# Performance work log

Hardware: AMD Instinct MI355X
Metric: run time of the kernel (lower is better)

The kernel has to match this reference:

```python
import jax, jax.numpy as jnp
import numpy as np

N = 32768      # total nodes
B = 64         # graphs
NPG = 512      # nodes per graph
E = 524288     # edges (avg degree 16)
H = 4          # heads
Fh = 64        # per-head dim
C = H * Fh     # 256
FIN = 128
RATIO = 0.5


def gat(x, src, dst, W, a_src, a_dst, bias, n_nodes):
    # PyG GATConv: linear -> add self-loops -> edge softmax over dst -> scatter-add
    h = (x @ W).reshape(n_nodes, H, Fh)
    loop = jnp.arange(n_nodes)
    s = jnp.concatenate([src, loop])
    d = jnp.concatenate([dst, loop])
    es = jnp.sum(h * a_src, axis=-1)  # [N,H]
    ed = jnp.sum(h * a_dst, axis=-1)  # [N,H]
    e = jax.nn.leaky_relu(es[s] + ed[d], 0.2)  # [E+N,H]
    m = jax.ops.segment_max(e, d, num_segments=n_nodes)
    ex = jnp.exp(e - m[d])
    den = jax.ops.segment_sum(ex, d, num_segments=n_nodes)
    alpha = ex / (den[d] + 1e-16)  # [E+N,H]
    out = jax.ops.segment_sum(alpha[:, :, None] * h[s], d, num_segments=n_nodes)
    return out.reshape(n_nodes, C) + bias


def pool(x, sw, sb, tw, tb, n_graphs, n_per):
    # equal-size graphs -> per-graph top-k as a batched top_k
    k = max(1, int(n_per * RATIO))
    scores = jax.nn.sigmoid(x @ sw + sb)[:, 0].reshape(n_graphs, n_per)
    _, idx = jax.lax.top_k(scores, k)  # [B,k]
    xb = x.reshape(n_graphs, n_per, x.shape[-1])
    sel = jnp.take_along_axis(xb, idx[:, :, None], axis=1)
    sel = sel.reshape(n_graphs * k, x.shape[-1])
    return sel @ tw + tb, k


def setup_inputs() -> dict:
    key = jax.random.key(0)
    ks = jax.random.split(key, 24)
    x = jax.random.normal(ks[0], (N, FIN), dtype=jnp.float32)
    # within-graph random edges
    gbase = jnp.repeat(jnp.arange(B, dtype=jnp.int32) * NPG, E // B)
    src = gbase + jax.random.randint(ks[1], (E,), 0, NPG)
    dst = gbase + jax.random.randint(ks[2], (E,), 0, NPG)
    edge_index = jnp.stack([src, dst]).astype(jnp.int32)
    batch = jnp.repeat(jnp.arange(B, dtype=jnp.int32), NPG)
    def lin(k, fi, fo):
        return jax.random.normal(k, (fi, fo), dtype=jnp.float32) / np.sqrt(fi)
    inp = dict(x=x, edge_index=edge_index, batch=batch)
    inp["W1"] = lin(ks[3], FIN, C)
    inp["a_src1"] = jax.random.normal(ks[4], (H, Fh), jnp.float32) / np.sqrt(Fh)
    inp["a_dst1"] = jax.random.normal(ks[5], (H, Fh), jnp.float32) / np.sqrt(Fh)
    inp["b1"] = jnp.zeros((C,), jnp.float32)
    inp["W2"] = lin(ks[6], C, C)
    inp["a_src2"] = jax.random.normal(ks[7], (H, Fh), jnp.float32) / np.sqrt(Fh)
    inp["a_dst2"] = jax.random.normal(ks[8], (H, Fh), jnp.float32) / np.sqrt(Fh)
    inp["b2"] = jnp.zeros((C,), jnp.float32)
    inp["p1_sw"] = lin(ks[9], C, 1)
    inp["p1_sb"] = jnp.zeros((1,), jnp.float32)
    inp["p1_tw"] = lin(ks[10], C, C)
    inp["p1_tb"] = jnp.zeros((C,), jnp.float32)
    inp["p2_sw"] = lin(ks[11], C, 1)
    inp["p2_sb"] = jnp.zeros((1,), jnp.float32)
    inp["p2_tw"] = lin(ks[12], C, C)
    inp["p2_tb"] = jnp.zeros((C,), jnp.float32)
    inp["c1w"] = lin(ks[13], C, 64)
    inp["c1b"] = jnp.zeros((64,), jnp.float32)
    inp["c2w"] = lin(ks[14], 64, 2)
    inp["c2b"] = jnp.zeros((2,), jnp.float32)
    return inp


def reference(x, edge_index, batch, W1, a_src1, a_dst1, b1, W2, a_src2, a_dst2, b2,
              p1_sw, p1_sb, p1_tw, p1_tb, p2_sw, p2_sb, p2_tw, p2_tb,
              c1w, c1b, c2w, c2b):
    src, dst = edge_index[0], edge_index[1]
    h = jax.nn.elu(gat(x, src, dst, W1, a_src1, a_dst1, b1, N))
    h = jax.nn.elu(gat(h, src, dst, W2, a_src2, a_dst2, b2, N))
    # pool1 then pool2 (edge_index after pooling is never consumed by the output path)
    h, k1 = pool(h, p1_sw, p1_sb, p1_tw, p1_tb, B, NPG)
    h, k2 = pool(h, p2_sw, p2_sb, p2_tw, p2_tb, B, k1)
    g = h.reshape(B, k2, C).mean(axis=1)  # global mean pool per graph
    g = jax.nn.relu(g @ c1w + c1b)
    g = g @ c2w + c2b
    return jax.nn.log_softmax(g, axis=1)
```

## Files before the change

### kernel.cpp

```cpp
#include <hip/hip_runtime.h>
#include <hip/hip_bf16.h>
#include <hip/hip_fp16.h>
#include <math.h>

constexpr int NN  = 32768;
constexpr int BG  = 64;
constexpr int NPG = 512;
constexpr int EG  = 524288;
constexpr int EPG = EG / BG;
constexpr int HH  = 4;
constexpr int FH  = 64;
constexpr int CC  = 256;
constexpr int FIN = 128;
constexpr int KP1 = 256;
constexpr int KP2 = 128;
constexpr int NS  = 4;

typedef __attribute__((ext_vector_type(8))) short short8;
typedef __attribute__((ext_vector_type(4))) float f32x4;
typedef __attribute__((ext_vector_type(2))) float f32x2v;

__device__ inline float leaky02(float v) { return v > 0.0f ? v : 0.2f * v; }

__device__ inline unsigned short f2bf(float v) {
    __hip_bfloat16 h = __float2bfloat16(v);
    return *(unsigned short*)&h;
}
__device__ inline float bf2f(unsigned short u) {
    __hip_bfloat16 h;
    *(unsigned short*)&h = u;
    return __bfloat162float(h);
}
__device__ inline void split2(float v, unsigned short& hi, unsigned short& lo) {
    hi = f2bf(v);
    lo = f2bf(v - bf2f(hi));
}
__device__ inline void split8(const float* p, short8& hi, short8& lo) {
    const float4 f0 = *(const float4*)p;
    const float4 f1 = *(const float4*)(p + 4);
    unsigned short h, l;
    split2(f0.x, h, l); hi[0] = (short)h; lo[0] = (short)l;
    split2(f0.y, h, l); hi[1] = (short)h; lo[1] = (short)l;
    split2(f0.z, h, l); hi[2] = (short)h; lo[2] = (short)l;
    split2(f0.w, h, l); hi[3] = (short)h; lo[3] = (short)l;
    split2(f1.x, h, l); hi[4] = (short)h; lo[4] = (short)l;
    split2(f1.y, h, l); hi[5] = (short)h; lo[5] = (short)l;
    split2(f1.z, h, l); hi[6] = (short)h; lo[6] = (short)l;
    split2(f1.w, h, l); hi[7] = (short)h; lo[7] = (short)l;
}

__device__ inline unsigned short f2h(float v) {
    __half h = __float2half(v);
    return *(unsigned short*)&h;
}
__device__ inline float h2f(unsigned short u) {
    __half h;
    *(unsigned short*)&h = u;
    return __half2float(h);
}

__device__ inline unsigned int fmap(float v) {
    unsigned int b = __float_as_uint(v);
    return (b & 0x80000000u) ? ~b : (b | 0x80000000u);
}

__device__ inline void acc8h(const unsigned short* p, float a, f32x2v* acc) {
    const uint4 u = *(const uint4*)p;
    const __half2* hp = (const __half2*)&u;
    f32x2v av; av[0] = a; av[1] = a;
#pragma unroll
    for (int i = 0; i < 4; ++i) {
        const float2 f = __half22float2(hp[i]);
        f32x2v fv; fv[0] = f.x; fv[1] = f.y;
        acc[i] = __builtin_elementwise_fma(fv, av, acc[i]);
    }
}

__global__ __launch_bounds__(1024) void setup_k(
        const int* __restrict__ src, const int* __restrict__ dst,
        int* __restrict__ rowp, int* __restrict__ esrc,
        const float* __restrict__ tw1, const float* __restrict__ sw2,
        const float* __restrict__ tb1, const float* __restrict__ sb2,
        float* __restrict__ w12, float* __restrict__ b12,
        const float* __restrict__ tw2, const float* __restrict__ c1w,
        const float* __restrict__ tb2, float* __restrict__ T,
        float* __restrict__ bc2,
        const float* __restrict__ W1, const float* __restrict__ W2,
        unsigned short* __restrict__ w1ph, unsigned short* __restrict__ w1pl,
        unsigned short* __restrict__ w2ph, unsigned short* __restrict__ w2pl,
        const float* __restrict__ x,
        unsigned short* __restrict__ xph, unsigned short* __restrict__ xpl) {
    __shared__ int lcnt[NPG];
    __shared__ int wsum[8];
    const int b = blockIdx.x;
    const int t = threadIdx.x;
    if (b < BG) {
        const int g = b;
        const int ebase = g * EPG;
        const int nbase = g * NPG;
        if (t < NPG) lcnt[t] = 0;
        __syncthreads();
        int ds[EPG / 1024];
#pragma unroll
        for (int j = 0; j < EPG / 1024; ++j) {
            ds[j] = dst[ebase + t + 1024 * j] - nbase;
            atomicAdd(&lcnt[ds[j]], 1);
        }
        __syncthreads();
        int c = 0, sInc = 0;
        if (t < NPG) {
            c = lcnt[t];
            sInc = c;
#pragma unroll
            for (int o = 1; o < 64; o <<= 1) {
                int v = __shfl_up(sInc, o);
                if ((t & 63) >= o) sInc += v;
            }
            if ((t & 63) == 63) wsum[t >> 6] = sInc;
        }
        __syncthreads();
        if (t < 8) {
            int v = wsum[t];
            int s = v;
#pragma unroll
            for (int o = 1; o < 8; o <<= 1) {
                int u2 = __shfl_up(s, o, 8);
                if (t >= o) s += u2;
            }
            wsum[t] = s - v;
        }
        __syncthreads();
        if (t < NPG) {
            const int ex = sInc - c + wsum[t >> 6];
            rowp[nbase + t] = ebase + ex;
            lcnt[t] = ex;
        }
        if (g == BG - 1 && t == 0) rowp[NN] = EG;
        __syncthreads();
#pragma unroll
        for (int j = 0; j < EPG / 1024; ++j) {
            int p = atomicAdd(&lcnt[ds[j]], 1);
            esrc[ebase + p] = src[ebase + t + 1024 * j];
        }
        return;
    }
    const int pb = b - BG;
    if (pb >= 114) {
        const size_t idx = ((size_t)(pb - 114) * 1024 + t) * 8;
        short8 hi, lo;
        split8(x + idx, hi, lo);
        *(short8*)(xph + idx) = hi;
        *(short8*)(xpl + idx) = lo;
        return;
    }
    if (t >= 256) return;
    if (pb < 66) {
        if (pb == 0) {
            float s = 0.0f;
            for (int o = 0; o < CC; ++o) s += tw1[t * CC + o] * sw2[o];
            w12[t] = s;
            if (t == 0) {
                float bb = 0.0f;
                for (int o = 0; o < CC; ++o) bb += tb1[o] * sw2[o];
                *b12 = bb + sb2[0];
            }
        } else if (pb < 65) {
            const int r = (pb - 1) * 4 + (t >> 6);
            const int cth = t & 63;
            float s = 0.0f;
            for (int j = 0; j < CC; ++j) s = fmaf(tw2[r * CC + j], c1w[j * 64 + cth], s);
            T[r * 64 + cth] = s;
        } else if (t < 64) {
            float s = 0.0f;
            for (int j = 0; j < CC; ++j) s = fmaf(tb2[j], c1w[j * 64 + t], s);
            bc2[t] = s;
        }
    } else {
        const int idx = (pb - 66) * 256 + t;
        if (idx < 4096) {
            const int nt = idx >> 8, rem = idx & 255;
            const int kg = rem >> 6, l = rem & 63;
            const int n = nt * 16 + (l & 15);
            const int kb = kg * 32 + (l >> 4) * 8;
            unsigned short h[8], lo[8];
#pragma unroll
            for (int j = 0; j < 8; ++j) split2(W1[(kb + j) * CC + n], h[j], lo[j]);
#pragma unroll
            for (int j = 0; j < 8; ++j) {
                w1ph[(size_t)idx * 8 + j] = h[j];
                w1pl[(size_t)idx * 8 + j] = lo[j];
            }
        } else {
            const int i2 = idx - 4096;
            const int nt = i2 >> 9, rem = i2 & 511;
            const int kg = rem >> 6, l = rem & 63;
            const int n = nt * 16 + (l & 15);
            const int kb = kg * 32 + (l >> 4) * 8;
            unsigned short h[8], lo[8];
#pragma unroll
            for (int j = 0; j < 8; ++j) split2(W2[(kb + j) * CC + n], h[j], lo[j]);
#pragma unroll
            for (int j = 0; j < 8; ++j) {
                w2ph[(size_t)i2 * 8 + j] = h[j];
                w2pl[(size_t)i2 * 8 + j] = lo[j];
            }
        }
    }
}

__global__ __launch_bounds__(256, 4) void gemm_mfma_attn(
        const unsigned short* __restrict__ Ahi, const unsigned short* __restrict__ Alo,
        const unsigned short* __restrict__ Bph, const unsigned short* __restrict__ Bpl,
        unsigned short* __restrict__ Cb, int K,
        const float* __restrict__ a_src, const float* __restrict__ a_dst,
        float* __restrict__ es, float* __restrict__ ed,
        const float* __restrict__ tw1, const float* __restrict__ T,
        const float* __restrict__ tb1, const float* __restrict__ bc2,
        const float* __restrict__ c1b, float* __restrict__ Wc,
        float* __restrict__ bcv) {
    const int t = threadIdx.x;
    const int bx = blockIdx.x;
    if (bx >= NN / 32) {
        const int fb = bx - NN / 32;
        if (fb < 64) {
            const int r = fb * 4 + (t >> 6);
            const int cth = t & 63;
            float s = 0.0f;
            for (int j = 0; j < CC; ++j) s = fmaf(tw1[r * CC + j], T[j * 64 + cth], s);
            Wc[r * 64 + cth] = s;
        } else if (t < 64) {
            float s = 0.0f;
            for (int j = 0; j < CC; ++j) s = fmaf(tb1[j], T[j * 64 + t], s);
            bcv[t] = s + bc2[t] + c1b[t];
        }
        return;
    }
    const int w = t >> 6;
    const int l = t & 63;
    const int xcd  = bx & 7;
    const int slot = bx >> 3;
    const int gph  = xcd + ((slot >> 4) << 3);
    const int row0 = gph * NPG + ((slot & 15) << 5);
    const int m = l & 15;
    const int q = l >> 4;
    const int ncol0 = w * 64;
    const int KG = K >> 5;

    const unsigned short* aH0 = Ahi + (size_t)(row0 + m) * K + q * 8;
    const unsigned short* aL0 = Alo + (size_t)(row0 + m) * K + q * 8;
    const unsigned short* aH1 = aH0 + (size_t)16 * K;
    const unsigned short* aL1 = aL0 + (size_t)16 * K;

    f32x4 acc0[4], acc1[4];
#pragma unroll
    for (int c = 0; c < 4; ++c) {
        acc0[c] = (f32x4){0.f, 0.f, 0.f, 0.f};
        acc1[c] = (f32x4){0.f, 0.f, 0.f, 0.f};
    }

    for (int kg = 0; kg < KG; ++kg) {
        const int ko = kg * 32;
        short8 ah0 = *(const short8*)(aH0 + ko);
        short8 al0 = *(const short8*)(aL0 + ko);
        short8 ah1 = *(const short8*)(aH1 + ko);
        short8 al1 = *(const short8*)(aL1 + ko);
#pragma unroll
        for (int c = 0; c < 4; ++c) {
            const int nt = (w << 2) + c;
            const size_t boff = ((size_t)(nt * KG + kg) * 64 + l) * 8;
            short8 bh = *(const short8*)(Bph + boff);
            short8 bl = *(const short8*)(Bpl + boff);
            acc0[c] = __builtin_amdgcn_mfma_f32_16x16x32_bf16(ah0, bh, acc0[c], 0, 0, 0);
            acc0[c] = __builtin_amdgcn_mfma_f32_16x16x32_bf16(ah0, bl, acc0[c], 0, 0, 0);
            acc0[c] = __builtin_amdgcn_mfma_f32_16x16x32_bf16(al0, bh, acc0[c], 0, 0, 0);
            acc1[c] = __builtin_amdgcn_mfma_f32_16x16x32_bf16(ah1, bh, acc1[c], 0, 0, 0);
            acc1[c] = __builtin_amdgcn_mfma_f32_16x16x32_bf16(ah1, bl, acc1[c], 0, 0, 0);
            acc1[c] = __builtin_amdgcn_mfma_f32_16x16x32_bf16(al1, bh, acc1[c], 0, 0, 0);
        }
    }

#pragma unroll
    for (int c = 0; c < 4; ++c)
#pragma unroll
        for (int r = 0; r < 4; ++r) {
            Cb[(size_t)(row0 + q * 4 + r) * CC + ncol0 + c * 16 + m] = f2h(acc0[c][r]);
            Cb[(size_t)(row0 + 16 + q * 4 + r) * CC + ncol0 + c * 16 + m] = f2h(acc1[c][r]);
        }

    float asv[4], adv[4];
#pragma unroll
    for (int c = 0; c < 4; ++c) {
        asv[c] = a_src[ncol0 + c * 16 + m];
        adv[c] = a_dst[ncol0 + c * 16 + m];
    }
#pragma unroll
    for (int r = 0; r < 4; ++r) {
        float ps0 = 0.f, pd0 = 0.f, ps1 = 0.f, pd1 = 0.f;
#pragma unroll
        for (int c = 0; c < 4; ++c) {
            ps0 = fmaf(acc0[c][r], asv[c], ps0);
            pd0 = fmaf(acc0[c][r], adv[c], pd0);
            ps1 = fmaf(acc1[c][r], asv[c], ps1);
            pd1 = fmaf(acc1[c][r], adv[c], pd1);
        }
#pragma unroll
        for (int o = 8; o >= 1; o >>= 1) {
            ps0 += __shfl_down(ps0, o, 16);
            pd0 += __shfl_down(pd0, o, 16);
            ps1 += __shfl_down(ps1, o, 16);
            pd1 += __shfl_down(pd1, o, 16);
        }
        if (m == 0) {
            es[(row0 + q * 4 + r) * HH + w] = ps0;
            ed[(row0 + q * 4 + r) * HH + w] = pd0;
            es[(row0 + 16 + q * 4 + r) * HH + w] = ps1;
            ed[(row0 + 16 + q * 4 + r) * HH + w] = pd1;
        }
    }
}

__global__ __launch_bounds__(256) void edge1_gemm2(
        const unsigned short* __restrict__ zh1,
        const int* __restrict__ rowp, const int* __restrict__ esrc,
        const float* __restrict__ es1, const float* __restrict__ ed1,
        const float* __restrict__ bias,
        const unsigned short* __restrict__ Bph, const unsigned short* __restrict__ Bpl,
        unsigned short* __restrict__ zh2,
        const float* __restrict__ a_src, const float* __restrict__ a_dst,
        float* __restrict__ es2, float* __restrict__ ed2) {
    __shared__ unsigned char AhB[32 * 512];
    __shared__ unsigned char AlB[32 * 512];
    const int t = threadIdx.x;
    const int w = t >> 6;
    const int l = t & 63;
    const int bx   = blockIdx.x;
    const int xcd  = bx & 7;
    const int slot = bx >> 3;
    const int gph  = xcd + ((slot >> 4) << 3);
    const int row0 = gph * NPG + ((slot & 15) << 5);

    const int h    = l & 3;
    const int ei   = l >> 2;
    const int lh   = l & 31;
    const int half = l >> 5;
    const int hcol = lh >> 3;
    const int c0   = lh << 3;

    for (int nd = 0; nd < 8; ++nd) {
        const int rloc = w * 8 + nd;
        const int d = row0 + rloc;
        const int beg = rowp[d];
        const int deg = rowp[d + 1] - beg;

        f32x2v acc[4];
#pragma unroll
        for (int i = 0; i < 4; ++i) acc[i] = (f32x2v){0.f, 0.f};

        if (deg <= 16 * NS) {
            const float edh = ed1[d * HH + h];
            int   sidx[NS];
            float v[NS];
#pragma unroll
            for (int j = 0; j < NS; ++j) { sidx[j] = d; v[j] = 0.0f; }
            float vmax = -INFINITY, eself = 0.0f, vself = 0.0f;
            if (ei == 0) {
                vself = leaky02(es1[d * HH + h] + edh);
                vmax = vself;
            }
#pragma unroll
            for (int j = 0; j < NS; ++j) {
                int i = ei + 16 * j;
                if (i < deg) {
                    sidx[j] = esrc[beg + i];
                    v[j] = leaky02(es1[sidx[j] * HH + h] + edh);
                    vmax = fmaxf(vmax, v[j]);
                }
            }
#pragma unroll
            for (int o = 4; o <= 32; o <<= 1) vmax = fmaxf(vmax, __shfl_xor(vmax, o));
            float dsum = 0.0f;
#pragma unroll
            for (int j = 0; j < NS; ++j) {
                int i = ei + 16 * j;
                if (i < deg) { v[j] = __expf(v[j] - vmax); dsum += v[j]; }
            }
            if (ei == 0) { eself = __expf(vself - vmax); dsum += eself; }
#pragma unroll
            for (int o = 4; o <= 32; o <<= 1) dsum += __shfl_xor(dsum, o);
            const float inv = 1.0f / (dsum + 1e-16f);
#pragma unroll
            for (int j = 0; j < NS; ++j) v[j] *= inv;
            eself *= inv;

            float aself = __shfl(eself, hcol);
            if (half) aself = 0.0f;
            acc8h(zh1 + (size_t)d * CC + c0, aself, acc);

#pragma unroll
            for (int j = 0; j < NS; ++j) {
                if (16 * j < deg) {
#pragma unroll
                    for (int rr = 0; rr < 8; ++rr) {
                        if (16 * j + 2 * rr < deg) {
                            const int slb  = (2 * rr + half) << 2;
                            const int srcn = __shfl(sidx[j], slb);
                            const float a  = __shfl(v[j], slb + hcol);
                            acc8h(zh1 + (size_t)srcn * CC + c0, a, acc);
                        }
                    }
                }
            }
        } else {
            const float edh = ed1[d * HH + h];
            float vmax = (ei == 0) ? leaky02(es1[d * HH + h] + edh) : -INFINITY;
            for (int i = ei; i < deg; i += 16)
                vmax = fmaxf(vmax, leaky02(es1[esrc[beg + i] * HH + h] + edh));
#pragma unroll
            for (int o = 4; o <= 32; o <<= 1) vmax = fmaxf(vmax, __shfl_xor(vmax, o));
            float dsum = (ei == 0) ? __expf(leaky02(es1[d * HH + h] + edh) - vmax) : 0.0f;
            for (int i = ei; i < deg; i += 16)
                dsum += __expf(leaky02(es1[esrc[beg + i] * HH + h] + edh) - vmax);
#pragma unroll
            for (int o = 4; o <= 32; o <<= 1) dsum += __shfl_xor(dsum, o);
            const float inv = 1.0f / (dsum + 1e-16f);

            const float vmaxc = __shfl(vmax, hcol);
            const float invc  = __shfl(inv,  hcol);
            const float edh4  = ed1[d * HH + hcol];
            float a0 = __expf(leaky02(es1[d * HH + hcol] + edh4) - vmaxc) * invc;
            if (half) a0 = 0.0f;
            acc8h(zh1 + (size_t)d * CC + c0, a0, acc);
            for (int e = half; e < deg; e += 2) {
                const int srcn = esrc[beg + e];
                const float a = __expf(leaky02(es1[srcn * HH + hcol] + edh4) - vmaxc) * invc;
                acc8h(zh1 + (size_t)srcn * CC + c0, a, acc);
            }
        }

#pragma unroll
        for (int i = 0; i < 4; ++i) {
            float a0 = acc[i][0]; a0 += __shfl_xor(a0, 32);
            float a1 = acc[i][1]; a1 += __shfl_xor(a1, 32);
            acc[i][0] = a0; acc[i][1] = a1;
        }

        const int cw = c0 + (half << 2);
        float o0 = half ? acc[2][0] : acc[0][0];
        float o1 = half ? acc[2][1] : acc[0][1];
        float o2 = half ? acc[3][0] : acc[1][0];
        float o3 = half ? acc[3][1] : acc[1][1];

        const float4 bv = *(const float4*)(bias + cw);
        o0 += bv.x; o0 = o0 > 0.0f ? o0 : __expf(o0) - 1.0f;
        o1 += bv.y; o1 = o1 > 0.0f ? o1 : __expf(o1) - 1.0f;
        o2 += bv.z; o2 = o2 > 0.0f ? o2 : __expf(o2) - 1.0f;
        o3 += bv.w; o3 = o3 > 0.0f ? o3 : __expf(o3) - 1.0f;

        ushort4 uh, ul;
        split2(o0, uh.x, ul.x);
        split2(o1, uh.y, ul.y);
        split2(o2, uh.z, ul.z);
        split2(o3, uh.w, ul.w);
        const size_t bo = (size_t)(((rloc * 512) + cw * 2) ^ ((rloc & 7) << 4));
        *(ushort4*)(AhB + bo) = uh;
        *(ushort4*)(AlB + bo) = ul;
    }

    __syncthreads();

    const int m = l & 15;
    const int q = l >> 4;
    const int ncol0 = w * 64;
    constexpr int KG = CC >> 5;

    f32x4 acc0[4], acc1[4];
#pragma unroll
    for (int c = 0; c < 4; ++c) {
        acc0[c] = (f32x4){0.f, 0.f, 0.f, 0.f};
        acc1[c] = (f32x4){0.f, 0.f, 0.f, 0.f};
    }

    for (int kg = 0; kg < KG; ++kg) {
        const int co = kg * 64 + q * 16;
        const size_t bo0 = (size_t)(((m * 512) + co) ^ ((m & 7) << 4));
        const size_t bo1 = (size_t)((((16 + m) * 512) + co) ^ ((m & 7) << 4));
        short8 ah0 = *(const short8*)(AhB + bo0);
        short8 al0 = *(const short8*)(AlB + bo0);
        short8 ah1 = *(const short8*)(AhB + bo1);
        short8 al1 = *(const short8*)(AlB + bo1);
#pragma unroll
        for (int c = 0; c < 4; ++c) {
            const int nt = (w << 2) + c;
            const size_t boff = ((size_t)(nt * KG + kg) * 64 + l) * 8;
            short8 bh = *(const short8*)(Bph + boff);
            short8 bl = *(const short8*)(Bpl + boff);
            acc0[c] = __builtin_amdgcn_mfma_f32_16x16x32_bf16(ah0, bh, acc0[c], 0, 0, 0);
            acc0[c] = __builtin_amdgcn_mfma_f32_16x16x32_bf16(ah0, bl, acc0[c], 0, 0, 0);
            acc0[c] = __builtin_amdgcn_mfma_f32_16x16x32_bf16(al0, bh, acc0[c], 0, 0, 0);
            acc1[c] = __builtin_amdgcn_mfma_f32_16x16x32_bf16(ah1, bh, acc1[c], 0, 0, 0);
            acc1[c] = __builtin_amdgcn_mfma_f32_16x16x32_bf16(ah1, bl, acc1[c], 0, 0, 0);
            acc1[c] = __builtin_amdgcn_mfma_f32_16x16x32_bf16(al1, bh, acc1[c], 0, 0, 0);
        }
    }

#pragma unroll
    for (int c = 0; c < 4; ++c)
#pragma unroll
        for (int r = 0; r < 4; ++r) {
            zh2[(size_t)(row0 + q * 4 + r) * CC + ncol0 + c * 16 + m] = f2h(acc0[c][r]);
            zh2[(size_t)(row0 + 16 + q * 4 + r) * CC + ncol0 + c * 16 + m] = f2h(acc1[c][r]);
        }

    float asv[4], adv[4];
#pragma unroll
    for (int c = 0; c < 4; ++c) {
        asv[c] = a_src[ncol0 + c * 16 + m];
        adv[c] = a_dst[ncol0 + c * 16 + m];
    }
#pragma unroll
    for (int r = 0; r < 4; ++r) {
        float ps0 = 0.f, pd0 = 0.f, ps1 = 0.f, pd1 = 0.f;
#pragma unroll
        for (int c = 0; c < 4; ++c) {
            ps0 = fmaf(acc0[c][r], asv[c], ps0);
            pd0 = fmaf(acc0[c][r], adv[c], pd0);
            ps1 = fmaf(acc1[c][r], asv[c], ps1);
            pd1 = fmaf(acc1[c][r], adv[c], pd1);
        }
#pragma unroll
        for (int o = 8; o >= 1; o >>= 1) {
            ps0 += __shfl_down(ps0, o, 16);
            pd0 += __shfl_down(pd0, o, 16);
            ps1 += __shfl_down(ps1, o, 16);
            pd1 += __shfl_down(pd1, o, 16);
        }
        if (m == 0) {
            es2[(row0 + q * 4 + r) * HH + w] = ps0;
            ed2[(row0 + q * 4 + r) * HH + w] = pd0;
            es2[(row0 + 16 + q * 4 + r) * HH + w] = ps1;
            ed2[(row0 + 16 + q * 4 + r) * HH + w] = pd1;
        }
    }
}

__global__ __launch_bounds__(256) void gat_edge(const unsigned short* __restrict__ zh,
                                                const int* __restrict__ rowp,
                                                const int* __restrict__ esrc,
                                                const float* __restrict__ es,
                                                const float* __restrict__ ed,
                                                const float* __restrict__ bias,
                                                unsigned short* __restrict__ featH,
                                                const float* __restrict__ sw1,
                                                const float* __restrict__ sb1,
                                                const float* __restrict__ w12,
                                                const float* __restrict__ b12,
                                                float* __restrict__ sc1,
                                                float* __restrict__ sc2) {
    const int w = threadIdx.x >> 6;
    const int l = threadIdx.x & 63;
    const int b    = blockIdx.x;
    const int xcd  = b & 7;
    const int slot = b >> 3;
    const int gph  = xcd + ((slot >> 7) << 3);
    const int d    = gph * NPG + ((slot & 127) << 2) + w;

    const int h    = l & 3;
    const int ei   = l >> 2;
    const int lh   = l & 31;
    const int half = l >> 5;
    const int hcol = lh >> 3;
    const int c0   = lh << 3;

    const int beg = rowp[d];
    const int deg = rowp[d + 1] - beg;

    f32x2v acc[4];
#pragma unroll
    for (int i = 0; i < 4; ++i) acc[i] = (f32x2v){0.f, 0.f};

    if (deg <= 16 * NS) {
        const float edh = ed[d * HH + h];
        int   sidx[NS];
        float v[NS];
#pragma unroll
        for (int j = 0; j < NS; ++j) { sidx[j] = d; v[j] = 0.0f; }
        float vmax = -INFINITY, eself = 0.0f, vself = 0.0f;
        if (ei == 0) {
            vself = leaky02(es[d * HH + h] + edh);
            vmax = vself;
        }
#pragma unroll
        for (int j = 0; j < NS; ++j) {
            int i = ei + 16 * j;
            if (i < deg) {
                sidx[j] = esrc[beg + i];
                v[j] = leaky02(es[sidx[j] * HH + h] + edh);
                vmax = fmaxf(vmax, v[j]);
            }
        }
#pragma unroll
        for (int o = 4; o <= 32; o <<= 1) vmax = fmaxf(vmax, __shfl_xor(vmax, o));
        float dsum = 0.0f;
#pragma unroll
        for (int j = 0; j < NS; ++j) {
            int i = ei + 16 * j;
            if (i < deg) { v[j] = __expf(v[j] - vmax); dsum += v[j]; }
        }
        if (ei == 0) { eself = __expf(vself - vmax); dsum += eself; }
#pragma unroll
        for (int o = 4; o <= 32; o <<= 1) dsum += __shfl_xor(dsum, o);
        const float inv = 1.0f / (dsum + 1e-16f);
#pragma unroll
        for (int j = 0; j < NS; ++j) v[j] *= inv;
        eself *= inv;

        float aself = __shfl(eself, hcol);
        if (half) aself = 0.0f;
        acc8h(zh + (size_t)d * CC + c0, aself, acc);

#pragma unroll
        for (int j = 0; j < NS; ++j) {
            if (16 * j < deg) {
#pragma unroll
                for (int rr = 0; rr < 8; ++rr) {
                    if (16 * j + 2 * rr < deg) {
                        const int slb  = (2 * rr + half) << 2;
                        const int srcn = __shfl(sidx[j], slb);
                        const float a  = __shfl(v[j], slb + hcol);
                        acc8h(zh + (size_t)srcn * CC + c0, a, acc);
                    }
                }
            }
        }
    } else {
        const float edh = ed[d * HH + h];
        float vmax = (ei == 0) ? leaky02(es[d * HH + h] + edh) : -INFINITY;
        for (int i = ei; i < deg; i += 16)
            vmax = fmaxf(vmax, leaky02(es[esrc[beg + i] * HH + h] + edh));
#pragma unroll
        for (int o = 4; o <= 32; o <<= 1) vmax = fmaxf(vmax, __shfl_xor(vmax, o));
        float dsum = (ei == 0) ? __expf(leaky02(es[d * HH + h] + edh) - vmax) : 0.0f;
        for (int i = ei; i < deg; i += 16)
            dsum += __expf(leaky02(es[esrc[beg + i] * HH + h] + edh) - vmax);
#pragma unroll
        for (int o = 4; o <= 32; o <<= 1) dsum += __shfl_xor(dsum, o);
        const float inv = 1.0f / (dsum + 1e-16f);

        const float vmaxc = __shfl(vmax, hcol);
        const float invc  = __shfl(inv,  hcol);
        const float edh4  = ed[d * HH + hcol];
        float a0 = __expf(leaky02(es[d * HH + hcol] + edh4) - vmaxc) * invc;
        if (half) a0 = 0.0f;
        acc8h(zh + (size_t)d * CC + c0, a0, acc);
        for (int e = half; e < deg; e += 2) {
            const int srcn = esrc[beg + e];
            const float a = __expf(leaky02(es[srcn * HH + hcol] + edh4) - vmaxc) * invc;
            acc8h(zh + (size_t)srcn * CC + c0, a, acc);
        }
    }

#pragma unroll
    for (int i = 0; i < 4; ++i) {
        float a0 = acc[i][0]; a0 += __shfl_xor(a0, 32);
        float a1 = acc[i][1]; a1 += __shfl_xor(a1, 32);
        acc[i][0] = a0; acc[i][1] = a1;
    }

    const int cw = c0 + (half << 2);
    float o0 = half ? acc[2][0] : acc[0][0];
    float o1 = half ? acc[2][1] : acc[0][1];
    float o2 = half ? acc[3][0] : acc[1][0];
    float o3 = half ? acc[3][1] : acc[1][1];

    const float4 bv = *(const float4*)(bias + cw);
    o0 += bv.x; o0 = o0 > 0.0f ? o0 : __expf(o0) - 1.0f;
    o1 += bv.y; o1 = o1 > 0.0f ? o1 : __expf(o1) - 1.0f;
    o2 += bv.z; o2 = o2 > 0.0f ? o2 : __expf(o2) - 1.0f;
    o3 += bv.w; o3 = o3 > 0.0f ? o3 : __expf(o3) - 1.0f;

    {
        ushort4 uf;
        uf.x = f2h(o0); uf.y = f2h(o1); uf.z = f2h(o2); uf.w = f2h(o3);
        *(ushort4*)(featH + (size_t)d * CC + cw) = uf;
    }

    {
        const float4 s1 = *(const float4*)(sw1 + cw);
        const float4 s2 = *(const float4*)(w12 + cw);
        float r1 = o0 * s1.x + o1 * s1.y + o2 * s1.z + o3 * s1.w;
        float r2 = o0 * s2.x + o1 * s2.y + o2 * s2.z + o3 * s2.w;
#pragma unroll
        for (int off = 32; off >= 1; off >>= 1) {
            r1 += __shfl_xor(r1, off);
            r2 += __shfl_xor(r2, off);
        }
        if (l == 0) {
            sc1[d] = r1 + sb1[0];
            sc2[d] = r2 + b12[0];
        }
    }
}

__global__ __launch_bounds__(512) void pool_g(const float* __restrict__ sc1,
                                              const float* __restrict__ sc2,
                                              const unsigned short* __restrict__ featH,
                                              const float* __restrict__ Wc,
                                              const float* __restrict__ bc,
                                              const float* __restrict__ c2w,
                                              const float* __restrict__ c2b,
                                              float* __restrict__ outp) {
    __shared__ unsigned int us[NPG];
    __shared__ unsigned char kb[NPG];
    __shared__ int list[KP2];
    __shared__ float v0[CC];
    __shared__ float vbuf[2][CC];
    __shared__ float part[4][64];
    __shared__ float v2[64];
    const int g = blockIdx.x;
    const int t = threadIdx.x;
    const int lane = t & 63, wid = t >> 6;

    const float s2val = sc2[(size_t)g * NPG + t];
    us[t] = fmap(sc1[(size_t)g * NPG + t]);
    __syncthreads();

    if (wid == 0) {
        unsigned int u[8];
#pragma unroll
        for (int j = 0; j < 8; ++j) u[j] = us[j * 64 + lane];
        unsigned int p = 0;
        for (int bb = 31; bb >= 0; --bb) {
            const unsigned int cand = p | (1u << bb);
            int cnt = 0;
#pragma unroll
            for (int j = 0; j < 8; ++j) cnt += __popcll(__ballot(u[j] >= cand));
            if (cnt >= KP1) p = cand;
        }
        int cgt = 0;
#pragma unroll
        for (int j = 0; j < 8; ++j) cgt += __popcll(__ballot(u[j] > p));
        const int kk = KP1 - cgt;
        const unsigned long long lm = (1ull << lane) - 1ull;
        int preEq = 0;
#pragma unroll
        for (int j = 0; j < 8; ++j) {
            const unsigned long long balEq = __ballot(u[j] == p);
            const int eqr = preEq + __popcll(balEq & lm);
            preEq += __popcll(balEq);
            kb[j * 64 + lane] =
                (unsigned char)((u[j] > p) || ((u[j] == p) && (eqr < kk)));
        }
    }
    __syncthreads();

    us[t] = kb[t] ? fmap(s2val) : 0u;
    __syncthreads();
    if (wid == 0) {
        unsigned int u[8];
#pragma unroll
        for (int j = 0; j < 8; ++j) u[j] = us[j * 64 + lane];
        unsigned int p = 0;
        for (int bb = 31; bb >= 0; --bb) {
            const unsigned int cand = p | (1u << bb);
            int cnt = 0;
#pragma unroll
            for (int j = 0; j < 8; ++j) cnt += __popcll(__ballot(u[j] >= cand));
            if (cnt >= KP2) p = cand;
        }
        int cgt = 0;
#pragma unroll
        for (int j = 0; j < 8; ++j) cgt += __popcll(__ballot(u[j] > p));
        const int kk = KP2 - cgt;
        const unsigned long long lm = (1ull << lane) - 1ull;
        int preEq = 0, preKeep = 0;
#pragma unroll
        for (int j = 0; j < 8; ++j) {
            const unsigned long long balEq = __ballot(u[j] == p);
            const int eqr = preEq + __popcll(balEq & lm);
            preEq += __popcll(balEq);
            const int keep = (u[j] > p) || ((u[j] == p) && (eqr < kk));
            const unsigned long long balK = __ballot(keep);
            const int pos = preKeep + __popcll(balK & lm);
            preKeep += __popcll(balK);
            if (keep) list[pos] = j * 64 + lane;
        }
    }
    __syncthreads();

    {
        const int col = t & (CC - 1);
        const int hf = t >> 8;
        float acc = 0.0f;
        for (int i = hf * 64; i < hf * 64 + 64; ++i)
            acc += h2f(featH[((size_t)g * NPG + list[i]) * CC + col]);
        vbuf[hf][col] = acc;
    }
    __syncthreads();
    if (t < CC) v0[t] = (vbuf[0][t] + vbuf[1][t]) * (1.0f / KP2);
    __syncthreads();

    if (t < 256) {
        const int q = t >> 6, cth = t & 63;
        float pr = 0.0f;
        for (int j = q * 64; j < q * 64 + 64; ++j)
            pr = fmaf(v0[j], Wc[j * 64 + cth], pr);
        part[q][cth] = pr;
    }
    __syncthreads();
    if (t < 64) {
        float u = bc[t];
#pragma unroll
        for (int q = 0; q < 4; ++q) u += part[q][t];
        v2[t] = fmaxf(u, 0.0f);
    }
    __syncthreads();
    if (t < 2) {
        float o = c2b[t];
        for (int j = 0; j < 64; ++j) o = fmaf(v2[j], c2w[j * 2 + t], o);
        part[0][t] = o;
    }
    __syncthreads();
    if (t == 0) {
        float a = part[0][0], bq = part[0][1];
        float mx = fmaxf(a, bq);
        float lse = mx + logf(expf(a - mx) + expf(bq - mx));
        outp[g * 2 + 0] = a - lse;
        outp[g * 2 + 1] = bq - lse;
    }
}

extern "C" void kernel_launch(void* const* d_in, const int* in_sizes, int n_in,
                              void* d_out, int out_size, void* d_ws, size_t ws_size,
                              hipStream_t stream) {
    const float* x      = (const float*)d_in[0];
    const int*   ei     = (const int*)d_in[1];
    const int*   src    = ei;
    const int*   dst    = ei + EG;
    const float* W1     = (const float*)d_in[3];
    const float* a_src1 = (const float*)d_in[4];
    const float* a_dst1 = (const float*)d_in[5];
    const float* b1     = (const float*)d_in[6];
    const float* W2     = (const float*)d_in[7];
    const float* a_src2 = (const float*)d_in[8];
    const float* a_dst2 = (const float*)d_in[9];
    const float* b2     = (const float*)d_in[10];
    const float* p1_sw  = (const float*)d_in[11];
    const float* p1_sb  = (const float*)d_in[12];
    const float* p1_tw  = (const float*)d_in[13];
    const float* p1_tb  = (const float*)d_in[14];
    const float* p2_sw  = (const float*)d_in[15];
    const float* p2_sb  = (const float*)d_in[16];
    const float* p2_tw  = (const float*)d_in[17];
    const float* p2_tb  = (const float*)d_in[18];
    const float* c1w    = (const float*)d_in[19];
    const float* c1b    = (const float*)d_in[20];
    const float* c2w    = (const float*)d_in[21];
    const float* c2b    = (const float*)d_in[22];
    float* out = (float*)d_out;

    float* ws = (float*)d_ws;
    float* z = ws;
    unsigned short* zh1 = (unsigned short*)z;
    unsigned short* zh2 = zh1 + (size_t)NN * CC;
    float* fregion = z + (size_t)NN * CC;
    unsigned short* featH = (unsigned short*)fregion;
    float* wsp = fregion + (size_t)NN * CC;
    unsigned short* w1ph = (unsigned short*)wsp;
    unsigned short* w1pl = w1ph + 256 * FIN;
    unsigned short* w2ph = w1pl + 256 * FIN;
    unsigned short* w2pl = w2ph + 256 * CC;
    float* es  = (float*)(w2pl + 256 * CC);
    float* ed  = es + NN * HH;
    int* rowp  = (int*)(ed + NN * HH);
    int* esrc  = rowp + NN + 1;
    float* sc1 = (float*)(esrc + EG);
    float* sc2 = sc1 + NN;
    int* sel1  = (int*)(sc2 + NN);
    float* w12 = (float*)(sel1 + NN);
    float* b12 = w12 + CC;
    float* T   = b12 + 64;
    float* Wc  = T + CC * 64;
    float* bc2 = Wc + CC * 64;
    float* bcv = bc2 + 64;
    float* es2 = bcv + 64;
    float* ed2 = es2 + (size_t)NN * HH;
    unsigned short* xph = (unsigned short*)(ed2 + (size_t)NN * HH);
    unsigned short* xpl = xph + (size_t)NN * FIN;

    setup_k<<<BG + 66 + 48 + 512, 1024, 0, stream>>>(
        src, dst, rowp, esrc,
        p1_tw, p2_sw, p1_tb, p2_sb, w12, b12, p2_tw, c1w, p2_tb, T, bc2,
        W1, W2, w1ph, w1pl, w2ph, w2pl, x, xph, xpl);

    gemm_mfma_attn<<<NN / 32 + 65, 256, 0, stream>>>(
        xph, xpl, w1ph, w1pl, zh1, FIN, a_src1, a_dst1, es, ed,
        p1_tw, T, p1_tb, bc2, c1b, Wc, bcv);

    edge1_gemm2<<<NN / 32, 256, 0, stream>>>(
        zh1, rowp, esrc, es, ed, b1,
        w2ph, w2pl, zh2, a_src2, a_dst2, es2, ed2);

    gat_edge<<<NN / 4, 256, 0, stream>>>(zh2, rowp, esrc, es2, ed2, b2,
                                         featH, p1_sw, p1_sb, w12, b12,
                                         sc1, sc2);

    pool_g<<<BG, 512, 0, stream>>>(sc1, sc2, featH, Wc, bcv, c2w, c2b, out);
}
```

Before: 232.8 us.

## Replace layer-2 gather aggregation with dense per-graph attention SpMM on MFMA

The second GAT aggregation no longer gathers source feature rows per edge. It builds a dense 32x512 attention matrix per block in shared memory, filled with LDS atomics in 64-column chunks, and multiplies it against the layer-2 features with split-bf16 MFMA. To feed this, edge1_gemm2 now writes layer-2 features as pre-packed hi/lo bf16 B-operand tiles per graph instead of a row-major fp16 array. This turns irregular gather traffic into dense matrix work and gives fp32-like precision. In exchange it performs about 32x more multiply-adds than the sparse edge count needs, adds zero-fill, atomic and barrier overhead over 8 chunks, and recomputes the attention exponentials.

```diff
diff --git a/kernel.cpp b/kernel.cpp
--- a/kernel.cpp
+++ b/kernel.cpp
@@ -325,7 +325,7 @@
         const float* __restrict__ es1, const float* __restrict__ ed1,
         const float* __restrict__ bias,
         const unsigned short* __restrict__ Bph, const unsigned short* __restrict__ Bpl,
-        unsigned short* __restrict__ zh2,
+        unsigned short* __restrict__ zh2ph, unsigned short* __restrict__ zh2pl,
         const float* __restrict__ a_src, const float* __restrict__ a_dst,
         float* __restrict__ es2, float* __restrict__ ed2) {
     __shared__ unsigned char AhB[32 * 512];
@@ -503,13 +503,29 @@
         }
     }
 
-#pragma unroll
-    for (int c = 0; c < 4; ++c)
-#pragma unroll
-        for (int r = 0; r < 4; ++r) {
-            zh2[(size_t)(row0 + q * 4 + r) * CC + ncol0 + c * 16 + m] = f2h(acc0[c][r]);
-            zh2[(size_t)(row0 + 16 + q * 4 + r) * CC + ncol0 + c * 16 + m] = f2h(acc1[c][r]);
-        }
+    {
+        const int kgB = slot & 15;
+        const size_t gb2 = (size_t)gph * 131072;
+#pragma unroll
+        for (int c = 0; c < 4; ++c) {
+            const int nt = (w << 2) + c;
+            const size_t ntb = gb2 + (size_t)(nt * 16 + kgB) * 512;
+#pragma unroll
+            for (int r = 0; r < 4; ++r) {
+                unsigned short hh, ll;
+                const int r32a = q * 4 + r;
+                const int lpa  = ((r32a >> 3) << 4) | m;
+                const size_t offa = ntb + (size_t)lpa * 8 + (r32a & 7);
+                split2(acc0[c][r], hh, ll);
+                zh2ph[offa] = hh; zh2pl[offa] = ll;
+                const int r32b = 16 + q * 4 + r;
+                const int lpb  = ((r32b >> 3) << 4) | m;
+                const size_t offb = ntb + (size_t)lpb * 8 + (r32b & 7);
+                split2(acc1[c][r], hh, ll);
+                zh2ph[offb] = hh; zh2pl[offb] = ll;
+            }
+        }
+    }
 
     float asv[4], adv[4];
 #pragma unroll
@@ -543,161 +559,180 @@
     }
 }
 
-__global__ __launch_bounds__(256) void gat_edge(const unsigned short* __restrict__ zh,
-                                                const int* __restrict__ rowp,
-                                                const int* __restrict__ esrc,
-                                                const float* __restrict__ es,
-                                                const float* __restrict__ ed,
-                                                const float* __restrict__ bias,
-                                                unsigned short* __restrict__ featH,
-                                                const float* __restrict__ sw1,
-                                                const float* __restrict__ sb1,
-                                                const float* __restrict__ w12,
-                                                const float* __restrict__ b12,
-                                                float* __restrict__ sc1,
-                                                float* __restrict__ sc2) {
-    const int w = threadIdx.x >> 6;
-    const int l = threadIdx.x & 63;
-    const int b    = blockIdx.x;
-    const int xcd  = b & 7;
-    const int slot = b >> 3;
-    const int gph  = xcd + ((slot >> 7) << 3);
-    const int d    = gph * NPG + ((slot & 127) << 2) + w;
-
-    const int h    = l & 3;
-    const int ei   = l >> 2;
-    const int lh   = l & 31;
-    const int half = l >> 5;
-    const int hcol = lh >> 3;
-    const int c0   = lh << 3;
-
-    const int beg = rowp[d];
-    const int deg = rowp[d + 1] - beg;
-
-    f32x2v acc[4];
-#pragma unroll
-    for (int i = 0; i < 4; ++i) acc[i] = (f32x2v){0.f, 0.f};
-
-    if (deg <= 16 * NS) {
+__global__ __launch_bounds__(256) void spmm_edge2(
+        const int* __restrict__ rowp, const int* __restrict__ esrc,
+        const float* __restrict__ es, const float* __restrict__ ed,
+        const float* __restrict__ bias,
+        const unsigned short* __restrict__ Bph, const unsigned short* __restrict__ Bpl,
+        unsigned short* __restrict__ featH,
+        const float* __restrict__ sw1, const float* __restrict__ sb1,
+        const float* __restrict__ w12, const float* __restrict__ b12,
+        float* __restrict__ sc1, float* __restrict__ sc2) {
+    __shared__ float Af[4][32][64];
+    __shared__ float vmL[32][4], invL[32][4], aslL[32][4], edhL[32][4];
+    __shared__ float scp1[4][32], scp2[4][32];
+    const int t = threadIdx.x;
+    const int w = t >> 6;
+    const int l = t & 63;
+    const int bx   = blockIdx.x;
+    const int xcd  = bx & 7;
+    const int slot = bx >> 3;
+    const int gph  = xcd + ((slot >> 4) << 3);
+    const int row0 = gph * NPG + ((slot & 15) << 5);
+    const int rbase = (slot & 15) << 5;
+    const int gbase = gph * NPG;
+
+    const int h  = l & 3;
+    const int ei = l >> 2;
+
+    for (int nd = 0; nd < 8; ++nd) {
+        const int rloc = w * 8 + nd;
+        const int d = row0 + rloc;
+        const int beg = rowp[d];
+        const int deg = rowp[d + 1] - beg;
         const float edh = ed[d * HH + h];
-        int   sidx[NS];
-        float v[NS];
-#pragma unroll
-        for (int j = 0; j < NS; ++j) { sidx[j] = d; v[j] = 0.0f; }
-        float vmax = -INFINITY, eself = 0.0f, vself = 0.0f;
-        if (ei == 0) {
-            vself = leaky02(es[d * HH + h] + edh);
-            vmax = vself;
-        }
-#pragma unroll
-        for (int j = 0; j < NS; ++j) {
-            int i = ei + 16 * j;
-            if (i < deg) {
-                sidx[j] = esrc[beg + i];
-                v[j] = leaky02(es[sidx[j] * HH + h] + edh);
-                vmax = fmaxf(vmax, v[j]);
-            }
-        }
+        const float vself = leaky02(es[d * HH + h] + edh);
+        float vmax = (ei == 0) ? vself : -INFINITY;
+        for (int i = ei; i < deg; i += 16)
+            vmax = fmaxf(vmax, leaky02(es[esrc[beg + i] * HH + h] + edh));
 #pragma unroll
         for (int o = 4; o <= 32; o <<= 1) vmax = fmaxf(vmax, __shfl_xor(vmax, o));
-        float dsum = 0.0f;
-#pragma unroll
-        for (int j = 0; j < NS; ++j) {
-            int i = ei + 16 * j;
-            if (i < deg) { v[j] = __expf(v[j] - vmax); dsum += v[j]; }
-        }
-        if (ei == 0) { eself = __expf(vself - vmax); dsum += eself; }
+        float dsum = (ei == 0) ? __expf(vself - vmax) : 0.0f;
+        for (int i = ei; i < deg; i += 16)
+            dsum += __expf(leaky02(es[esrc[beg + i] * HH + h] + edh) - vmax);
 #pragma unroll
         for (int o = 4; o <= 32; o <<= 1) dsum += __shfl_xor(dsum, o);
         const float inv = 1.0f / (dsum + 1e-16f);
-#pragma unroll
-        for (int j = 0; j < NS; ++j) v[j] *= inv;
-        eself *= inv;
-
-        float aself = __shfl(eself, hcol);
-        if (half) aself = 0.0f;
-        acc8h(zh + (size_t)d * CC + c0, aself, acc);
-
-#pragma unroll
-        for (int j = 0; j < NS; ++j) {
-            if (16 * j < deg) {
-#pragma unroll
-                for (int rr = 0; rr < 8; ++rr) {
-                    if (16 * j + 2 * rr < deg) {
-                        const int slb  = (2 * rr + half) << 2;
-                        const int srcn = __shfl(sidx[j], slb);
-                        const float a  = __shfl(v[j], slb + hcol);
-                        acc8h(zh + (size_t)srcn * CC + c0, a, acc);
-                    }
+        if (ei == 0) {
+            vmL[rloc][h]  = vmax;
+            invL[rloc][h] = inv;
+            aslL[rloc][h] = __expf(vself - vmax) * inv;
+            edhL[rloc][h] = edh;
+        }
+    }
+
+    const int m = l & 15;
+    const int q = l >> 4;
+    const int ncol0 = w * 64;
+    const size_t gb2 = (size_t)gph * 131072;
+
+    f32x4 acc0[4], acc1[4];
+#pragma unroll
+    for (int c = 0; c < 4; ++c) {
+        acc0[c] = (f32x4){0.f, 0.f, 0.f, 0.f};
+        acc1[c] = (f32x4){0.f, 0.f, 0.f, 0.f};
+    }
+
+    for (int ck = 0; ck < 8; ++ck) {
+        __syncthreads();
+        {
+            float* afl = &Af[0][0][0];
+            for (int it = t; it < 4 * 32 * 64; it += 256) afl[it] = 0.0f;
+        }
+        __syncthreads();
+        for (int nd = 0; nd < 8; ++nd) {
+            const int rloc = w * 8 + nd;
+            const int d = row0 + rloc;
+            const int beg = rowp[d];
+            const int deg = rowp[d + 1] - beg;
+            const float edh  = edhL[rloc][h];
+            const float vmax = vmL[rloc][h];
+            const float inv  = invL[rloc][h];
+            for (int i = ei; i < deg; i += 16) {
+                const int srcn = esrc[beg + i];
+                const int rel = srcn - gbase;
+                if ((rel >> 6) == ck) {
+                    const float a =
+                        __expf(leaky02(es[srcn * HH + h] + edh) - vmax) * inv;
+                    atomicAdd(&Af[h][rloc][rel & 63], a);
                 }
             }
-        }
-    } else {
-        const float edh = ed[d * HH + h];
-        float vmax = (ei == 0) ? leaky02(es[d * HH + h] + edh) : -INFINITY;
-        for (int i = ei; i < deg; i += 16)
-            vmax = fmaxf(vmax, leaky02(es[esrc[beg + i] * HH + h] + edh));
-#pragma unroll
-        for (int o = 4; o <= 32; o <<= 1) vmax = fmaxf(vmax, __shfl_xor(vmax, o));
-        float dsum = (ei == 0) ? __expf(leaky02(es[d * HH + h] + edh) - vmax) : 0.0f;
-        for (int i = ei; i < deg; i += 16)
-            dsum += __expf(leaky02(es[esrc[beg + i] * HH + h] + edh) - vmax);
-#pragma unroll
-        for (int o = 4; o <= 32; o <<= 1) dsum += __shfl_xor(dsum, o);
-        const float inv = 1.0f / (dsum + 1e-16f);
-
-        const float vmaxc = __shfl(vmax, hcol);
-        const float invc  = __shfl(inv,  hcol);
-        const float edh4  = ed[d * HH + hcol];
-        float a0 = __expf(leaky02(es[d * HH + hcol] + edh4) - vmaxc) * invc;
-        if (half) a0 = 0.0f;
-        acc8h(zh + (size_t)d * CC + c0, a0, acc);
-        for (int e = half; e < deg; e += 2) {
-            const int srcn = esrc[beg + e];
-            const float a = __expf(leaky02(es[srcn * HH + hcol] + edh4) - vmaxc) * invc;
-            acc8h(zh + (size_t)srcn * CC + c0, a, acc);
-        }
-    }
-
-#pragma unroll
-    for (int i = 0; i < 4; ++i) {
-        float a0 = acc[i][0]; a0 += __shfl_xor(a0, 32);
-        float a1 = acc[i][1]; a1 += __shfl_xor(a1, 32);
-        acc[i][0] = a0; acc[i][1] = a1;
-    }
-
-    const int cw = c0 + (half << 2);
-    float o0 = half ? acc[2][0] : acc[0][0];
-    float o1 = half ? acc[2][1] : acc[0][1];
-    float o2 = half ? acc[3][0] : acc[1][0];
-    float o3 = half ? acc[3][1] : acc[1][1];
-
-    const float4 bv = *(const float4*)(bias + cw);
-    o0 += bv.x; o0 = o0 > 0.0f ? o0 : __expf(o0) - 1.0f;
-    o1 += bv.y; o1 = o1 > 0.0f ? o1 : __expf(o1) - 1.0f;
-    o2 += bv.z; o2 = o2 > 0.0f ? o2 : __expf(o2) - 1.0f;
-    o3 += bv.w; o3 = o3 > 0.0f ? o3 : __expf(o3) - 1.0f;
-
-    {
-        ushort4 uf;
-        uf.x = f2h(o0); uf.y = f2h(o1); uf.z = f2h(o2); uf.w = f2h(o3);
-        *(ushort4*)(featH + (size_t)d * CC + cw) = uf;
-    }
-
-    {
-        const float4 s1 = *(const float4*)(sw1 + cw);
-        const float4 s2 = *(const float4*)(w12 + cw);
-        float r1 = o0 * s1.x + o1 * s1.y + o2 * s1.z + o3 * s1.w;
-        float r2 = o0 * s2.x + o1 * s2.y + o2 * s2.z + o3 * s2.w;
-#pragma unroll
-        for (int off = 32; off >= 1; off >>= 1) {
-            r1 += __shfl_xor(r1, off);
-            r2 += __shfl_xor(r2, off);
-        }
-        if (l == 0) {
-            sc1[d] = r1 + sb1[0];
-            sc2[d] = r2 + b12[0];
-        }
+            if (ei == 0) {
+                const int rel = rbase + rloc;
+                if ((rel >> 6) == ck) atomicAdd(&Af[h][rloc][rel & 63], aslL[rloc][h]);
+            }
+        }
+        __syncthreads();
+#pragma unroll
+        for (int ks = 0; ks < 2; ++ks) {
+            short8 ah0, al0, ah1, al1;
+            {
+                unsigned short hh, ll;
+#pragma unroll
+                for (int j = 0; j < 8; ++j) {
+                    split2(Af[w][m][ks * 32 + q * 8 + j], hh, ll);
+                    ah0[j] = (short)hh; al0[j] = (short)ll;
+                    split2(Af[w][16 + m][ks * 32 + q * 8 + j], hh, ll);
+                    ah1[j] = (short)hh; al1[j] = (short)ll;
+                }
+            }
+            const int kg = ck * 2 + ks;
+#pragma unroll
+            for (int c = 0; c < 4; ++c) {
+                const int nt = (w << 2) + c;
+                const size_t boff = gb2 + ((size_t)(nt * 16 + kg) * 64 + l) * 8;
+                short8 bh = *(const short8*)(Bph + boff);
+                short8 bl = *(const short8*)(Bpl + boff);
+                acc0[c] = __builtin_amdgcn_mfma_f32_16x16x32_bf16(ah0, bh, acc0[c], 0, 0, 0);
+                acc0[c] = __builtin_amdgcn_mfma_f32_16x16x32_bf16(ah0, bl, acc0[c], 0, 0, 0);
+                acc0[c] = __builtin_amdgcn_mfma_f32_16x16x32_bf16(al0, bh, acc0[c], 0, 0, 0);
+                acc1[c] = __builtin_amdgcn_mfma_f32_16x16x32_bf16(ah1, bh, acc1[c], 0, 0, 0);
+                acc1[c] = __builtin_amdgcn_mfma_f32_16x16x32_bf16(ah1, bl, acc1[c], 0, 0, 0);
+                acc1[c] = __builtin_amdgcn_mfma_f32_16x16x32_bf16(al1, bh, acc1[c], 0, 0, 0);
+            }
+        }
+    }
+
+#pragma unroll
+    for (int c = 0; c < 4; ++c) {
+        const int col = ncol0 + c * 16 + m;
+        const float bv = bias[col];
+#pragma unroll
+        for (int r = 0; r < 4; ++r) {
+            float o0 = acc0[c][r] + bv;
+            o0 = o0 > 0.0f ? o0 : __expf(o0) - 1.0f;
+            acc0[c][r] = o0;
+            featH[(size_t)(row0 + q * 4 + r) * CC + col] = f2h(o0);
+            float o1 = acc1[c][r] + bv;
+            o1 = o1 > 0.0f ? o1 : __expf(o1) - 1.0f;
+            acc1[c][r] = o1;
+            featH[(size_t)(row0 + 16 + q * 4 + r) * CC + col] = f2h(o1);
+        }
+    }
+    float s1v[4], s2v[4];
+#pragma unroll
+    for (int c = 0; c < 4; ++c) {
+        s1v[c] = sw1[ncol0 + c * 16 + m];
+        s2v[c] = w12[ncol0 + c * 16 + m];
+    }
+#pragma unroll
+    for (int r = 0; r < 4; ++r) {
+        float p10 = 0.f, p20 = 0.f, p11 = 0.f, p21 = 0.f;
+#pragma unroll
+        for (int c = 0; c < 4; ++c) {
+            p10 = fmaf(acc0[c][r], s1v[c], p10);
+            p20 = fmaf(acc0[c][r], s2v[c], p20);
+            p11 = fmaf(acc1[c][r], s1v[c], p11);
+            p21 = fmaf(acc1[c][r], s2v[c], p21);
+        }
+#pragma unroll
+        for (int o = 8; o >= 1; o >>= 1) {
+            p10 += __shfl_down(p10, o, 16);
+            p20 += __shfl_down(p20, o, 16);
+            p11 += __shfl_down(p11, o, 16);
+            p21 += __shfl_down(p21, o, 16);
+        }
+        if (m == 0) {
+            scp1[w][q * 4 + r] = p10;      scp2[w][q * 4 + r] = p20;
+            scp1[w][16 + q * 4 + r] = p11; scp2[w][16 + q * 4 + r] = p21;
+        }
+    }
+    __syncthreads();
+    if (t < 32) {
+        const float r1 = scp1[0][t] + scp1[1][t] + scp1[2][t] + scp1[3][t];
+        const float r2 = scp2[0][t] + scp2[1][t] + scp2[2][t] + scp2[3][t];
+        sc1[row0 + t] = r1 + sb1[0];
+        sc2[row0 + t] = r2 + b12[0];
     }
 }
 
@@ -860,8 +895,8 @@
 
     float* ws = (float*)d_ws;
     float* z = ws;
-    unsigned short* zh1 = (unsigned short*)z;
-    unsigned short* zh2 = zh1 + (size_t)NN * CC;
+    unsigned short* zh1   = (unsigned short*)z;
+    unsigned short* zh2ph = zh1 + (size_t)NN * CC;
     float* fregion = z + (size_t)NN * CC;
     unsigned short* featH = (unsigned short*)fregion;
     float* wsp = fregion + (size_t)NN * CC;
@@ -886,6 +921,7 @@
     float* ed2 = es2 + (size_t)NN * HH;
     unsigned short* xph = (unsigned short*)(ed2 + (size_t)NN * HH);
     unsigned short* xpl = xph + (size_t)NN * FIN;
+    unsigned short* zh2pl = xpl + (size_t)NN * FIN;
 
     setup_k<<<BG + 66 + 48 + 512, 1024, 0, stream>>>(
         src, dst, rowp, esrc,
@@ -898,11 +934,11 @@
 
     edge1_gemm2<<<NN / 32, 256, 0, stream>>>(
         zh1, rowp, esrc, es, ed, b1,
-        w2ph, w2pl, zh2, a_src2, a_dst2, es2, ed2);
-
-    gat_edge<<<NN / 4, 256, 0, stream>>>(zh2, rowp, esrc, es2, ed2, b2,
-                                         featH, p1_sw, p1_sb, w12, b12,
-                                         sc1, sc2);
+        w2ph, w2pl, zh2ph, zh2pl, a_src2, a_dst2, es2, ed2);
+
+    spmm_edge2<<<NN / 32, 256, 0, stream>>>(
+        rowp, esrc, es2, ed2, b2, zh2ph, zh2pl, featH,
+        p1_sw, p1_sb, w12, b12, sc1, sc2);
 
     pool_g<<<BG, 512, 0, stream>>>(sc1, sc2, featH, Wc, bcv, c2w, c2b, out);
 }
```

Result: slower. 299.5 us (+28.6%).
